# Performance work log

Measured on AMD Instinct MI355X. Metric: run time of the kernel, lower is better.

The kernel has to match this reference:

```python
import jax, jax.numpy as jnp
import numpy as np

NUM_USERS = 500000
NUM_ITEMS = 500000
EMB_DIM = 64
BATCH = 16384
BN_EPS = 1e-5


def setup_inputs() -> dict:
    key = jax.random.key(0)
    ks = jax.random.split(key, 16)
    d = {}
    d["user_ids"] = jax.random.randint(ks[0], (BATCH,), 0, NUM_USERS)
    d["item_ids"] = jax.random.randint(ks[1], (BATCH,), 0, NUM_ITEMS)
    # wide layer: Linear(num_users+num_items, 1) -> weight stored as a flat vector + scalar bias
    d["wide_w"] = jax.random.normal(ks[2], (NUM_USERS + NUM_ITEMS,), jnp.float32) * 0.002
    d["wide_b"] = jnp.zeros((), jnp.float32)
    # embedding tables (init normal std=0.1 as in _init_weights)
    d["user_table"] = jax.random.normal(ks[3], (NUM_USERS, EMB_DIM), jnp.float32) * 0.1
    d["item_table"] = jax.random.normal(ks[4], (NUM_ITEMS, EMB_DIM), jnp.float32) * 0.1
    # deep MLP: 128 -> 256 -> 128 -> 64 -> 1, xavier-ish init, zero bias
    dims = [2 * EMB_DIM, 256, 128, 64]
    for i, (din, dout) in enumerate(zip(dims[:-1], dims[1:]), start=1):
        scale = float(np.sqrt(6.0 / (din + dout)))
        d[f"w{i}"] = jax.random.uniform(ks[4 + i], (din, dout), jnp.float32, -scale, scale)
        d[f"b{i}"] = jnp.zeros((dout,), jnp.float32)
        d[f"g{i}"] = jnp.ones((dout,), jnp.float32)   # BN gamma
        d[f"be{i}"] = jnp.zeros((dout,), jnp.float32)  # BN beta
    scale = float(np.sqrt(6.0 / (64 + 1)))
    d["w4"] = jax.random.uniform(ks[9], (64, 1), jnp.float32, -scale, scale)
    d["b4"] = jnp.zeros((1,), jnp.float32)
    return d


def _bn_eval(h, g, be):
    # eval-mode BatchNorm1d with running_mean=0, running_var=1
    return g * (h * (1.0 / jnp.sqrt(1.0 + BN_EPS))) + be


def reference(user_ids, item_ids, wide_w, wide_b, user_table, item_table,
              w1, b1, g1, be1, w2, b2, g2, be2, w3, b3, g3, be3, w4, b4):
    # Wide path: one_hot(user) @ W.T + one_hot(item) @ W.T + b  ==  gather + sum + bias
    wide = wide_w[user_ids] + wide_w[NUM_USERS + item_ids] + wide_b  # [B]
    # Deep path
    x = jnp.concatenate([user_table[user_ids], item_table[item_ids]], axis=1)  # [B, 128]
    for w, b, g, be in ((w1, b1, g1, be1), (w2, b2, g2, be2), (w3, b3, g3, be3)):
        x = _bn_eval(jax.nn.relu(x @ w + b), g, be)  # Linear -> ReLU -> BN (Dropout=id in eval)
    deep = (x @ w4 + b4)[:, 0]  # [B]
    return wide + deep
```

## Files before the change

kernel.cpp:

```cpp
#include <hip/hip_runtime.h>


#define NT 512
#define TS 32

constexpr int NUM_USERS = 500000;
constexpr float BN_INV = 0.9999950000374997f;

struct __align__(16) Smem {
    float xs[TS * 128];
    float h1[TS * 256];
    float wbuf[4096];
};

#define FMA4(xk, wv, a)                      \
    do {                                     \
        (a).x = fmaf((xk), (wv).x, (a).x);   \
        (a).y = fmaf((xk), (wv).y, (a).y);   \
        (a).z = fmaf((xk), (wv).z, (a).z);   \
        (a).w = fmaf((xk), (wv).w, (a).w);   \
    } while (0)

template <int K, int N>
__device__ __forceinline__ void mlp_layer(
    const float* __restrict__ w, const float* __restrict__ bias,
    const float* __restrict__ gamma, const float* __restrict__ beta,
    const float* in_lds, float* out_lds, float* wbuf, int t)
{
    constexpr int JG = N / 4;
    constexpr int S  = N / 64;
    constexpr int CK = 4096 / N;

    const int j0 = (t % JG) * 4;
    const int s0 = (t / JG) * S;

    float4 acc[S];
#pragma unroll
    for (int s = 0; s < S; ++s) acc[s] = make_float4(0.f, 0.f, 0.f, 0.f);

    for (int kc = 0; kc < K; kc += CK) {
        __syncthreads();
        {
            const float4* src = (const float4*)(w + kc * N);
            float4* dst = (float4*)wbuf;
            dst[t]       = src[t];
            dst[t + 512] = src[t + 512];
        }
        __syncthreads();

#pragma unroll
        for (int k4 = 0; k4 < CK; k4 += 4) {
            float4 xv[S];
#pragma unroll
            for (int s = 0; s < S; ++s)
                xv[s] = *(const float4*)&in_lds[(s0 + s) * K + kc + k4];
#pragma unroll
            for (int kk = 0; kk < 4; ++kk) {
                float4 wv = *(const float4*)&wbuf[(k4 + kk) * N + j0];
#pragma unroll
                for (int s = 0; s < S; ++s) {
                    float xk = (kk == 0) ? xv[s].x
                             : (kk == 1) ? xv[s].y
                             : (kk == 2) ? xv[s].z
                                         : xv[s].w;
                    FMA4(xk, wv, acc[s]);
                }
            }
        }
    }

    const float4 bv = *(const float4*)&bias[j0];
    const float4 gv = *(const float4*)&gamma[j0];
    const float4 ev = *(const float4*)&beta[j0];
#pragma unroll
    for (int s = 0; s < S; ++s) {
        float4 o;
        o.x = fmaxf(acc[s].x + bv.x, 0.f) * (gv.x * BN_INV) + ev.x;
        o.y = fmaxf(acc[s].y + bv.y, 0.f) * (gv.y * BN_INV) + ev.y;
        o.z = fmaxf(acc[s].z + bv.z, 0.f) * (gv.z * BN_INV) + ev.z;
        o.w = fmaxf(acc[s].w + bv.w, 0.f) * (gv.w * BN_INV) + ev.w;
        *(float4*)&out_lds[(s0 + s) * N + j0] = o;
    }
}

__global__ __launch_bounds__(NT) void wd_kernel(
    const int* __restrict__ user_ids, const int* __restrict__ item_ids,
    const float* __restrict__ wide_w, const float* __restrict__ wide_b,
    const float* __restrict__ user_table, const float* __restrict__ item_table,
    const float* __restrict__ w1, const float* __restrict__ b1,
    const float* __restrict__ g1, const float* __restrict__ be1,
    const float* __restrict__ w2, const float* __restrict__ b2,
    const float* __restrict__ g2, const float* __restrict__ be2,
    const float* __restrict__ w3, const float* __restrict__ b3,
    const float* __restrict__ g3, const float* __restrict__ be3,
    const float* __restrict__ w4, const float* __restrict__ b4,
    float* __restrict__ out)
{
    __shared__ Smem sm;
    const int t = threadIdx.x;
    const int sbase = blockIdx.x * TS;

    {
        const int s = t >> 4;
        const int p = t & 15;
        const int uid = user_ids[sbase + s];
        const int iid = item_ids[sbase + s];
        ((float4*)&sm.xs[s * 128])[p] =
            ((const float4*)(user_table + (long)uid * 64))[p];
        ((float4*)&sm.xs[s * 128])[16 + p] =
            ((const float4*)(item_table + (long)iid * 64))[p];
    }

    float widev = 0.0f;
    if (t < TS * 8 && (t & 7) == 0) {
        const int s = t >> 3;
        const int uid = user_ids[sbase + s];
        const int iid = item_ids[sbase + s];
        widev = wide_w[uid] + wide_w[NUM_USERS + iid] + wide_b[0];
    }

    mlp_layer<128, 256>(w1, b1, g1, be1, sm.xs, sm.h1, sm.wbuf, t);
    mlp_layer<256, 128>(w2, b2, g2, be2, sm.h1, sm.xs, sm.wbuf, t);
    mlp_layer<128, 64 >(w3, b3, g3, be3, sm.xs, sm.h1, sm.wbuf, t);
    __syncthreads();

    if (t < TS * 8) {
        const int s = t >> 3;
        const int g = t & 7;
        const float* h = &sm.h1[s * 64 + g * 8];
        const float4 ha = *(const float4*)(h);
        const float4 hb = *(const float4*)(h + 4);
        const float4 wa = *(const float4*)(w4 + g * 8);
        const float4 wb = *(const float4*)(w4 + g * 8 + 4);
        float p = ha.x * wa.x + ha.y * wa.y + ha.z * wa.z + ha.w * wa.w
                + hb.x * wb.x + hb.y * wb.y + hb.z * wb.z + hb.w * wb.w;
        p += __shfl_down(p, 4);
        p += __shfl_down(p, 2);
        p += __shfl_down(p, 1);
        if (g == 0) out[sbase + s] = widev + p + b4[0];
    }
}

extern "C" void kernel_launch(void* const* d_in, const int* in_sizes, int n_in,
                              void* d_out, int out_size, void* d_ws, size_t ws_size,
                              hipStream_t stream) {
    (void)in_sizes; (void)n_in; (void)d_ws; (void)ws_size;
    const int*   user_ids   = (const int*)d_in[0];
    const int*   item_ids   = (const int*)d_in[1];
    const float* wide_w     = (const float*)d_in[2];
    const float* wide_b     = (const float*)d_in[3];
    const float* user_table = (const float*)d_in[4];
    const float* item_table = (const float*)d_in[5];
    const float* w1 = (const float*)d_in[6];
    const float* b1 = (const float*)d_in[7];
    const float* g1 = (const float*)d_in[8];
    const float* be1 = (const float*)d_in[9];
    const float* w2 = (const float*)d_in[10];
    const float* b2 = (const float*)d_in[11];
    const float* g2 = (const float*)d_in[12];
    const float* be2 = (const float*)d_in[13];
    const float* w3 = (const float*)d_in[14];
    const float* b3 = (const float*)d_in[15];
    const float* g3 = (const float*)d_in[16];
    const float* be3 = (const float*)d_in[17];
    const float* w4 = (const float*)d_in[18];
    const float* b4 = (const float*)d_in[19];
    float* out = (float*)d_out;

    const int grid = 16384 / TS;
    wd_kernel<<<grid, NT, 0, stream>>>(
        user_ids, item_ids, wide_w, wide_b, user_table, item_table,
        w1, b1, g1, be1, w2, b2, g2, be2, w3, b3, g3, be3, w4, b4, out);
}
```

Baseline: 308.4 us.

## Read MLP weights directly from global memory instead of staging through LDS

Removes the LDS weight buffer and the chunked cooperative copies with their double barriers. Each thread now loads its float4 weight columns straight from global memory, relying on L2/L1 caching, and only needs one barrier between layers. LDS use drops from 64KB to 48KB per block, and launch_bounds asks for 4 blocks per CU to raise occupancy. The cost is redundant global/cache weight loads across threads that share columns, plus possible register pressure from the occupancy hint.

```diff
diff --git a/kernel.cpp b/kernel.cpp
--- a/kernel.cpp
+++ b/kernel.cpp
@@ -10,7 +10,6 @@
 struct __align__(16) Smem {
     float xs[TS * 128];
     float h1[TS * 256];
-    float wbuf[4096];
 };
 
 #define FMA4(xk, wv, a)                      \
@@ -25,11 +24,11 @@
 __device__ __forceinline__ void mlp_layer(
     const float* __restrict__ w, const float* __restrict__ bias,
     const float* __restrict__ gamma, const float* __restrict__ beta,
-    const float* in_lds, float* out_lds, float* wbuf, int t)
+    const float* in_lds, float* out_lds, int t)
 {
     constexpr int JG = N / 4;
     constexpr int S  = N / 64;
-    constexpr int CK = 4096 / N;
+    constexpr int NW = N / 4;
 
     const int j0 = (t % JG) * 4;
     const int s0 = (t / JG) * S;
@@ -38,34 +37,24 @@
 #pragma unroll
     for (int s = 0; s < S; ++s) acc[s] = make_float4(0.f, 0.f, 0.f, 0.f);
 
-    for (int kc = 0; kc < K; kc += CK) {
-        __syncthreads();
-        {
-            const float4* src = (const float4*)(w + kc * N);
-            float4* dst = (float4*)wbuf;
-            dst[t]       = src[t];
-            dst[t + 512] = src[t + 512];
-        }
-        __syncthreads();
+    const float4* wp = (const float4*)w + (j0 >> 2);
 
+#pragma unroll 4
+    for (int k4 = 0; k4 < K; k4 += 4) {
+        float4 wv0 = wp[(k4 + 0) * NW];
+        float4 wv1 = wp[(k4 + 1) * NW];
+        float4 wv2 = wp[(k4 + 2) * NW];
+        float4 wv3 = wp[(k4 + 3) * NW];
+        float4 xv[S];
 #pragma unroll
-        for (int k4 = 0; k4 < CK; k4 += 4) {
-            float4 xv[S];
+        for (int s = 0; s < S; ++s)
+            xv[s] = *(const float4*)&in_lds[(s0 + s) * K + k4];
 #pragma unroll
-            for (int s = 0; s < S; ++s)
-                xv[s] = *(const float4*)&in_lds[(s0 + s) * K + kc + k4];
-#pragma unroll
-            for (int kk = 0; kk < 4; ++kk) {
-                float4 wv = *(const float4*)&wbuf[(k4 + kk) * N + j0];
-#pragma unroll
-                for (int s = 0; s < S; ++s) {
-                    float xk = (kk == 0) ? xv[s].x
-                             : (kk == 1) ? xv[s].y
-                             : (kk == 2) ? xv[s].z
-                                         : xv[s].w;
-                    FMA4(xk, wv, acc[s]);
-                }
-            }
+        for (int s = 0; s < S; ++s) {
+            FMA4(xv[s].x, wv0, acc[s]);
+            FMA4(xv[s].y, wv1, acc[s]);
+            FMA4(xv[s].z, wv2, acc[s]);
+            FMA4(xv[s].w, wv3, acc[s]);
         }
     }
 
@@ -83,7 +72,7 @@
     }
 }
 
-__global__ __launch_bounds__(NT) void wd_kernel(
+__global__ __launch_bounds__(NT, 4) void wd_kernel(
     const int* __restrict__ user_ids, const int* __restrict__ item_ids,
     const float* __restrict__ wide_w, const float* __restrict__ wide_b,
     const float* __restrict__ user_table, const float* __restrict__ item_table,
@@ -118,10 +107,13 @@
         const int iid = item_ids[sbase + s];
         widev = wide_w[uid] + wide_w[NUM_USERS + iid] + wide_b[0];
     }
+    __syncthreads();
 
-    mlp_layer<128, 256>(w1, b1, g1, be1, sm.xs, sm.h1, sm.wbuf, t);
-    mlp_layer<256, 128>(w2, b2, g2, be2, sm.h1, sm.xs, sm.wbuf, t);
-    mlp_layer<128, 64 >(w3, b3, g3, be3, sm.xs, sm.h1, sm.wbuf, t);
+    mlp_layer<128, 256>(w1, b1, g1, be1, sm.xs, sm.h1, t);
+    __syncthreads();
+    mlp_layer<256, 128>(w2, b2, g2, be2, sm.h1, sm.xs, t);
+    __syncthreads();
+    mlp_layer<128, 64 >(w3, b3, g3, be3, sm.xs, sm.h1, t);
     __syncthreads();
 
     if (t < TS * 8) {
```

Measured after the change: 314.3 us. About the same (+1.9%).

## Use split-bf16 MFMA for MLP layers with pre-swizzled weight fragments

Applied to the files above, without the earlier changes.

Replaces the scalar-FMA fp32 MLP with bf16 MFMA 16x16x32 instructions. It uses a three-term hi/lo split (hh, hl, lh) to keep close to fp32 accuracy. A small prep kernel converts and swizzles w1-w3 into MFMA fragment layout in the workspace on each call. Activations are held in LDS as padded bf16 hi/lo pairs, and the block size drops to 256 threads. This removes the LDS weight staging and FMA-bound inner loops, at the cost of an extra launch, triple the MFMA work, and some lost precision.

```diff
diff --git a/kernel.cpp b/kernel.cpp
--- a/kernel.cpp
+++ b/kernel.cpp
@@ -1,139 +1,183 @@
 #include <hip/hip_runtime.h>
 
 
-#define NT 512
+#define NT 256
 #define TS 32
 
 constexpr int NUM_USERS = 500000;
 constexpr float BN_INV = 0.9999950000374997f;
 
+typedef float f32x4 __attribute__((ext_vector_type(4)));
+typedef short short8 __attribute__((ext_vector_type(8)));
+
+union U4S8 { uint4 u; short8 s; };
+
+__device__ __forceinline__ unsigned short f2bf(float x) {
+    unsigned u = __float_as_uint(x);
+    return (unsigned short)((u + 0x7fffu + ((u >> 16) & 1u)) >> 16);
+}
+__device__ __forceinline__ float bf2f(unsigned short h) {
+    return __uint_as_float(((unsigned)h) << 16);
+}
+
+__device__ __forceinline__ void split_store4(unsigned short* ph, unsigned short* pl, float4 v) {
+    unsigned short h0 = f2bf(v.x), h1 = f2bf(v.y), h2 = f2bf(v.z), h3 = f2bf(v.w);
+    unsigned short l0 = f2bf(v.x - bf2f(h0)), l1 = f2bf(v.y - bf2f(h1));
+    unsigned short l2 = f2bf(v.z - bf2f(h2)), l3 = f2bf(v.w - bf2f(h3));
+    uint2 hw, lw;
+    hw.x = (unsigned)h0 | ((unsigned)h1 << 16); hw.y = (unsigned)h2 | ((unsigned)h3 << 16);
+    lw.x = (unsigned)l0 | ((unsigned)l1 << 16); lw.y = (unsigned)l2 | ((unsigned)l3 << 16);
+    *(uint2*)ph = hw; *(uint2*)pl = lw;
+}
+
+__global__ __launch_bounds__(256) void wd_prep(
+    const float* __restrict__ w1, const float* __restrict__ w2,
+    const float* __restrict__ w3, uint4* __restrict__ ws)
+{
+    int tid = blockIdx.x * 256 + threadIdx.x;
+    if (tid >= 9216) return;
+    const float* W; int ncols, kt, fg, lane, hib, lob, idx;
+    if (tid < 4096)      { W = w1; ncols = 256; int r = tid;        kt = r >> 10; fg = (r >> 6) & 15; lane = r & 63; hib = 0;     lob = 4096;  idx = r; }
+    else if (tid < 8192) { W = w2; ncols = 128; int r = tid - 4096; kt = r >> 9;  fg = (r >> 6) & 7;  lane = r & 63; hib = 8192;  lob = 12288; idx = r; }
+    else                 { W = w3; ncols = 64;  int r = tid - 8192; kt = r >> 8;  fg = (r >> 6) & 3;  lane = r & 63; hib = 16384; lob = 17408; idx = r; }
+    const int q = lane >> 4, rr = lane & 15;
+    const int k0 = kt * 32 + q * 8;
+    const int n  = fg * 16 + rr;
+    unsigned short hs[8], ls[8];
+#pragma unroll
+    for (int j = 0; j < 8; ++j) {
+        float v = W[(k0 + j) * ncols + n];
+        unsigned short h = f2bf(v);
+        hs[j] = h;
+        ls[j] = f2bf(v - bf2f(h));
+    }
+    uint4 hu, lu;
+    hu.x = (unsigned)hs[0] | ((unsigned)hs[1] << 16); hu.y = (unsigned)hs[2] | ((unsigned)hs[3] << 16);
+    hu.z = (unsigned)hs[4] | ((unsigned)hs[5] << 16); hu.w = (unsigned)hs[6] | ((unsigned)hs[7] << 16);
+    lu.x = (unsigned)ls[0] | ((unsigned)ls[1] << 16); lu.y = (unsigned)ls[2] | ((unsigned)ls[3] << 16);
+    lu.z = (unsigned)ls[4] | ((unsigned)ls[5] << 16); lu.w = (unsigned)ls[6] | ((unsigned)ls[7] << 16);
+    ws[hib + idx] = hu;
+    ws[lob + idx] = lu;
+}
+
 struct __align__(16) Smem {
-    float xs[TS * 128];
-    float h1[TS * 256];
-    float wbuf[4096];
+    unsigned short xh[TS * 136], xl[TS * 136];
+    unsigned short yh[TS * 264], yl[TS * 264];
 };
 
-#define FMA4(xk, wv, a)                      \
-    do {                                     \
-        (a).x = fmaf((xk), (wv).x, (a).x);   \
-        (a).y = fmaf((xk), (wv).y, (a).y);   \
-        (a).z = fmaf((xk), (wv).z, (a).z);   \
-        (a).w = fmaf((xk), (wv).w, (a).w);   \
-    } while (0)
-
-template <int K, int N>
-__device__ __forceinline__ void mlp_layer(
-    const float* __restrict__ w, const float* __restrict__ bias,
-    const float* __restrict__ gamma, const float* __restrict__ beta,
-    const float* in_lds, float* out_lds, float* wbuf, int t)
+template <int K, int N, int SIN, int SOUT>
+__device__ __forceinline__ void mfma_layer(
+    const uint4* __restrict__ Ah, const uint4* __restrict__ Al,
+    const float* __restrict__ bias, const float* __restrict__ gamma,
+    const float* __restrict__ beta,
+    const unsigned short* inh, const unsigned short* inl,
+    unsigned short* outh, unsigned short* outl, int t)
 {
-    constexpr int JG = N / 4;
-    constexpr int S  = N / 64;
-    constexpr int CK = 4096 / N;
-
-    const int j0 = (t % JG) * 4;
-    const int s0 = (t / JG) * S;
-
-    float4 acc[S];
-#pragma unroll
-    for (int s = 0; s < S; ++s) acc[s] = make_float4(0.f, 0.f, 0.f, 0.f);
-
-    for (int kc = 0; kc < K; kc += CK) {
-        __syncthreads();
-        {
-            const float4* src = (const float4*)(w + kc * N);
-            float4* dst = (float4*)wbuf;
-            dst[t]       = src[t];
-            dst[t + 512] = src[t + 512];
-        }
-        __syncthreads();
-
-#pragma unroll
-        for (int k4 = 0; k4 < CK; k4 += 4) {
-            float4 xv[S];
-#pragma unroll
-            for (int s = 0; s < S; ++s)
-                xv[s] = *(const float4*)&in_lds[(s0 + s) * K + kc + k4];
-#pragma unroll
-            for (int kk = 0; kk < 4; ++kk) {
-                float4 wv = *(const float4*)&wbuf[(k4 + kk) * N + j0];
-#pragma unroll
-                for (int s = 0; s < S; ++s) {
-                    float xk = (kk == 0) ? xv[s].x
-                             : (kk == 1) ? xv[s].y
-                             : (kk == 2) ? xv[s].z
-                                         : xv[s].w;
-                    FMA4(xk, wv, acc[s]);
-                }
+    constexpr int KT = K / 32, FT = N / 64, FTOT = N / 16;
+    const int wave = t >> 6, lane = t & 63, q = lane >> 4, r = lane & 15;
+
+    f32x4 zero = {0.f, 0.f, 0.f, 0.f};
+    f32x4 acc[FT][2];
+#pragma unroll
+    for (int ft = 0; ft < FT; ++ft)
+#pragma unroll
+        for (int s = 0; s < 2; ++s) acc[ft][s] = zero;
+
+#pragma unroll
+    for (int kt = 0; kt < KT; ++kt) {
+        short8 bh[2], bl[2];
+#pragma unroll
+        for (int s = 0; s < 2; ++s) {
+            const int bi = (s * 16 + r) * SIN + kt * 32 + q * 8;
+            bh[s] = *(const short8*)&inh[bi];
+            bl[s] = *(const short8*)&inl[bi];
+        }
+#pragma unroll
+        for (int ft = 0; ft < FT; ++ft) {
+            const int fo = (kt * FTOT + wave * FT + ft) * 64 + lane;
+            U4S8 ah, al; ah.u = Ah[fo]; al.u = Al[fo];
+#pragma unroll
+            for (int s = 0; s < 2; ++s) {
+                acc[ft][s] = __builtin_amdgcn_mfma_f32_16x16x32_bf16(ah.s, bh[s], acc[ft][s], 0, 0, 0);
+                acc[ft][s] = __builtin_amdgcn_mfma_f32_16x16x32_bf16(ah.s, bl[s], acc[ft][s], 0, 0, 0);
+                acc[ft][s] = __builtin_amdgcn_mfma_f32_16x16x32_bf16(al.s, bh[s], acc[ft][s], 0, 0, 0);
             }
         }
     }
 
-    const float4 bv = *(const float4*)&bias[j0];
-    const float4 gv = *(const float4*)&gamma[j0];
-    const float4 ev = *(const float4*)&beta[j0];
-#pragma unroll
-    for (int s = 0; s < S; ++s) {
-        float4 o;
-        o.x = fmaxf(acc[s].x + bv.x, 0.f) * (gv.x * BN_INV) + ev.x;
-        o.y = fmaxf(acc[s].y + bv.y, 0.f) * (gv.y * BN_INV) + ev.y;
-        o.z = fmaxf(acc[s].z + bv.z, 0.f) * (gv.z * BN_INV) + ev.z;
-        o.w = fmaxf(acc[s].w + bv.w, 0.f) * (gv.w * BN_INV) + ev.w;
-        *(float4*)&out_lds[(s0 + s) * N + j0] = o;
-    }
-}
-
-__global__ __launch_bounds__(NT) void wd_kernel(
+#pragma unroll
+    for (int ft = 0; ft < FT; ++ft) {
+        const int f = (wave * FT + ft) * 16 + q * 4;
+        const float4 bv = *(const float4*)&bias[f];
+        const float4 gv = *(const float4*)&gamma[f];
+        const float4 ev = *(const float4*)&beta[f];
+#pragma unroll
+        for (int s = 0; s < 2; ++s) {
+            const int sample = s * 16 + r;
+            float4 o;
+            o.x = fmaxf(acc[ft][s][0] + bv.x, 0.f) * (gv.x * BN_INV) + ev.x;
+            o.y = fmaxf(acc[ft][s][1] + bv.y, 0.f) * (gv.y * BN_INV) + ev.y;
+            o.z = fmaxf(acc[ft][s][2] + bv.z, 0.f) * (gv.z * BN_INV) + ev.z;
+            o.w = fmaxf(acc[ft][s][3] + bv.w, 0.f) * (gv.w * BN_INV) + ev.w;
+            split_store4(&outh[sample * SOUT + f], &outl[sample * SOUT + f], o);
+        }
+    }
+}
+
+__global__ __launch_bounds__(NT) void wd_main(
     const int* __restrict__ user_ids, const int* __restrict__ item_ids,
     const float* __restrict__ wide_w, const float* __restrict__ wide_b,
     const float* __restrict__ user_table, const float* __restrict__ item_table,
-    const float* __restrict__ w1, const float* __restrict__ b1,
-    const float* __restrict__ g1, const float* __restrict__ be1,
-    const float* __restrict__ w2, const float* __restrict__ b2,
-    const float* __restrict__ g2, const float* __restrict__ be2,
-    const float* __restrict__ w3, const float* __restrict__ b3,
-    const float* __restrict__ g3, const float* __restrict__ be3,
+    const float* __restrict__ b1, const float* __restrict__ g1, const float* __restrict__ be1,
+    const float* __restrict__ b2, const float* __restrict__ g2, const float* __restrict__ be2,
+    const float* __restrict__ b3, const float* __restrict__ g3, const float* __restrict__ be3,
     const float* __restrict__ w4, const float* __restrict__ b4,
-    float* __restrict__ out)
+    const uint4* __restrict__ wsA, float* __restrict__ out)
 {
     __shared__ Smem sm;
     const int t = threadIdx.x;
     const int sbase = blockIdx.x * TS;
+    const int s = t >> 3, g = t & 7;
 
     {
-        const int s = t >> 4;
-        const int p = t & 15;
         const int uid = user_ids[sbase + s];
         const int iid = item_ids[sbase + s];
-        ((float4*)&sm.xs[s * 128])[p] =
-            ((const float4*)(user_table + (long)uid * 64))[p];
-        ((float4*)&sm.xs[s * 128])[16 + p] =
-            ((const float4*)(item_table + (long)iid * 64))[p];
-    }
-
-    float widev = 0.0f;
-    if (t < TS * 8 && (t & 7) == 0) {
-        const int s = t >> 3;
-        const int uid = user_ids[sbase + s];
-        const int iid = item_ids[sbase + s];
-        widev = wide_w[uid] + wide_w[NUM_USERS + iid] + wide_b[0];
-    }
-
-    mlp_layer<128, 256>(w1, b1, g1, be1, sm.xs, sm.h1, sm.wbuf, t);
-    mlp_layer<256, 128>(w2, b2, g2, be2, sm.h1, sm.xs, sm.wbuf, t);
-    mlp_layer<128, 64 >(w3, b3, g3, be3, sm.xs, sm.h1, sm.wbuf, t);
-    __syncthreads();
-
-    if (t < TS * 8) {
-        const int s = t >> 3;
-        const int g = t & 7;
-        const float* h = &sm.h1[s * 64 + g * 8];
-        const float4 ha = *(const float4*)(h);
-        const float4 hb = *(const float4*)(h + 4);
+        const float* src = (g < 4) ? user_table + (long)uid * 64 + g * 16
+                                   : item_table + (long)iid * 64 + (g - 4) * 16;
+#pragma unroll
+        for (int j = 0; j < 4; ++j) {
+            float4 v = ((const float4*)src)[j];
+            const int di = s * 136 + g * 16 + j * 4;
+            split_store4(&sm.xh[di], &sm.xl[di], v);
+        }
+    }
+    float widev = 0.f;
+    if (g == 0)
+        widev = wide_w[user_ids[sbase + s]] + wide_w[NUM_USERS + item_ids[sbase + s]] + wide_b[0];
+    __syncthreads();
+
+    mfma_layer<128, 256, 136, 264>(wsA,         wsA + 4096,  b1, g1, be1, sm.xh, sm.xl, sm.yh, sm.yl, t);
+    __syncthreads();
+    mfma_layer<256, 128, 264, 136>(wsA + 8192,  wsA + 12288, b2, g2, be2, sm.yh, sm.yl, sm.xh, sm.xl, t);
+    __syncthreads();
+    mfma_layer<128, 64, 136, 72>(wsA + 16384, wsA + 17408, b3, g3, be3, sm.xh, sm.xl, sm.yh, sm.yl, t);
+    __syncthreads();
+
+    {
+        const short8 hh = *(const short8*)&sm.yh[s * 72 + g * 8];
+        const short8 hl = *(const short8*)&sm.yl[s * 72 + g * 8];
         const float4 wa = *(const float4*)(w4 + g * 8);
         const float4 wb = *(const float4*)(w4 + g * 8 + 4);
-        float p = ha.x * wa.x + ha.y * wa.y + ha.z * wa.z + ha.w * wa.w
-                + hb.x * wb.x + hb.y * wb.y + hb.z * wb.z + hb.w * wb.w;
+        float h0 = bf2f((unsigned short)hh[0]) + bf2f((unsigned short)hl[0]);
+        float h1 = bf2f((unsigned short)hh[1]) + bf2f((unsigned short)hl[1]);
+        float h2 = bf2f((unsigned short)hh[2]) + bf2f((unsigned short)hl[2]);
+        float h3 = bf2f((unsigned short)hh[3]) + bf2f((unsigned short)hl[3]);
+        float h4 = bf2f((unsigned short)hh[4]) + bf2f((unsigned short)hl[4]);
+        float h5 = bf2f((unsigned short)hh[5]) + bf2f((unsigned short)hl[5]);
+        float h6 = bf2f((unsigned short)hh[6]) + bf2f((unsigned short)hl[6]);
+        float h7 = bf2f((unsigned short)hh[7]) + bf2f((unsigned short)hl[7]);
+        float p = h0 * wa.x + h1 * wa.y + h2 * wa.z + h3 * wa.w
+                + h4 * wb.x + h5 * wb.y + h6 * wb.z + h7 * wb.w;
         p += __shfl_down(p, 4);
         p += __shfl_down(p, 2);
         p += __shfl_down(p, 1);
@@ -144,7 +188,7 @@
 extern "C" void kernel_launch(void* const* d_in, const int* in_sizes, int n_in,
                               void* d_out, int out_size, void* d_ws, size_t ws_size,
                               hipStream_t stream) {
-    (void)in_sizes; (void)n_in; (void)d_ws; (void)ws_size;
+    (void)in_sizes; (void)n_in; (void)ws_size;
     const int*   user_ids   = (const int*)d_in[0];
     const int*   item_ids   = (const int*)d_in[1];
     const float* wide_w     = (const float*)d_in[2];
@@ -166,9 +210,11 @@
     const float* w4 = (const float*)d_in[18];
     const float* b4 = (const float*)d_in[19];
     float* out = (float*)d_out;
-
-    const int grid = 16384 / TS;
-    wd_kernel<<<grid, NT, 0, stream>>>(
+    uint4* ws = (uint4*)d_ws;
+
+    wd_prep<<<36, 256, 0, stream>>>(w1, w2, w3, ws);
+    wd_main<<<16384 / TS, NT, 0, stream>>>(
         user_ids, item_ids, wide_w, wide_b, user_table, item_table,
-        w1, b1, g1, be1, w2, b2, g2, be2, w3, b3, g3, be3, w4, b4, out);
-}
+        b1, g1, be1, b2, g2, be2, b3, g3, be3, w4, b4,
+        (const uint4*)ws, out);
+}
```

Result: faster. 260.5 us (-15.5%).
